# Kernel tuning notes

Hardware: AMD Instinct MI355X
Metric: run time of the kernel (lower is better)

Reference implementation:

```python
import jax, jax.numpy as jnp
import numpy as np

P = 64
K = 64
D = 2048
KERNEL_MUL = 2.0
KERNEL_NUM = 5


def setup_inputs() -> dict:
    key = jax.random.key(0)
    k1, k2 = jax.random.split(key)
    source = jax.random.normal(k1, (P * K, D), dtype=jnp.float32)
    target = jax.random.normal(k2, (P * K, D), dtype=jnp.float32)
    return {"source": source, "target": target}


def _mmd_terms(source, target):
    # split into P groups of K rows each, process all splits at once
    src = source.reshape(P, K, D)
    tgt = target.reshape(P, K, D)
    total = jnp.concatenate([src, tgt], axis=1)          # [P, 2K, D]
    n = 2 * K
    # pairwise squared L2 distances per split: [P, 2K, 2K]
    sq = jnp.sum(total * total, axis=-1)                  # [P, 2K]
    gram = jnp.einsum('pid,pjd->pij', total, total)       # [P, 2K, 2K]
    l2 = sq[:, :, None] + sq[:, None, :] - 2.0 * gram
    # bandwidth from detached distances (torch uses L2_distance.data)
    bw = jax.lax.stop_gradient(jnp.sum(l2, axis=(1, 2))) / (n * n - n)  # [P]
    bw = bw / (KERNEL_MUL ** (KERNEL_NUM // 2))
    mults = KERNEL_MUL ** jnp.arange(KERNEL_NUM, dtype=jnp.float32)     # [kn]
    bws = bw[:, None] * mults[None, :] + 1e-9                           # [P, kn]
    # multi-bandwidth Gaussian kernel sum: [P, 2K, 2K]
    kern = jnp.sum(jnp.exp(-l2[:, None, :, :] / bws[:, :, None, None]), axis=1)
    XX = kern[:, :K, :K]
    YY = kern[:, K:, K:]
    XY = kern[:, :K, K:]
    YX = kern[:, K:, :K]
    xx = jnp.mean(XX, axis=(1, 2))
    yy = jnp.mean(YY, axis=(1, 2))
    xy = jnp.mean(XY, axis=(1, 2))
    yx = jnp.mean(YX, axis=(1, 2))
    per_split_loss = xx + yy - xy - yx                    # [P]
    total_loss = jnp.sum(per_split_loss) / P
    return total_loss, l2, xx, yy, xy, yx


def reference(source, target):
    total_loss, l2, xx, yy, xy, yx = _mmd_terms(source, target)
    # original returns max of l2dist from the LAST split only
    max_l2_last = jnp.max(l2[-1])
    return (total_loss.reshape(1), max_l2_last,
            jnp.sum(xx) / P, jnp.sum(yy) / P, jnp.sum(xy) / P, jnp.sum(yx) / P)
```

## Files before the change

### kernel.cpp

```cpp
#include <hip/hip_runtime.h>

typedef _Float16 half8 __attribute__((ext_vector_type(8)));
typedef float floatx4 __attribute__((ext_vector_type(4)));
typedef unsigned int uint2v __attribute__((ext_vector_type(2)));

#define NSPLIT 64
#define KS 64
#define DIM 2048
#define NROW 128
#define BK 128
#define KSPL 8
#define KCH (DIM / KSPL)
#define NKC_A (KCH / BK)
#define SST 152
#define GSZ (NROW * NROW)
#define GT_OFF (NSPLIT * KSPL * GSZ)

__device__ __forceinline__ unsigned int pk16(float a, float b) {
  return __builtin_bit_cast(unsigned int, __builtin_amdgcn_cvt_pkrtz(a, b));
}

__global__ void init_kernel(float* out, float* ws) {
  if (threadIdx.x < 6) out[threadIdx.x] = 0.0f;
  if (threadIdx.x < NSPLIT) ws[GT_OFF + threadIdx.x] = 0.0f;
}

__global__ __launch_bounds__(1024) void gram_kernel(const float* __restrict__ src,
                                                    const float* __restrict__ tgt,
                                                    float* __restrict__ ws) {
  __shared__ __align__(16) _Float16 stage[NROW * SST];
  __shared__ float red[16];

  const int p = blockIdx.x >> 3;
  const int c = blockIdx.x & (KSPL - 1);
  const int tid = threadIdx.x;
  const int lane = tid & 63;
  const int wave = tid >> 6;

  const int srow = tid >> 3;
  const int c4 = (tid & 7) * 4;
  const float* rowp = ((srow < KS) ? (src + (size_t)(p * KS + srow) * DIM)
                                   : (tgt + (size_t)(p * KS + (srow - KS)) * DIM)) +
                      c * KCH;

  const int wr = (wave >> 2) * 32;
  const int wc = (wave & 3) * 32;
  const int fr = lane & 15;
  const int fk = (lane >> 4) * 8;

  floatx4 acc00 = {0.f, 0.f, 0.f, 0.f};
  floatx4 acc01 = {0.f, 0.f, 0.f, 0.f};
  floatx4 acc10 = {0.f, 0.f, 0.f, 0.f};
  floatx4 acc11 = {0.f, 0.f, 0.f, 0.f};

  float4 f0, f1, f2, f3;
#define LOADK(kc)                                      \
  do {                                                 \
    const float* gp_ = rowp + (kc) * BK + c4;          \
    f0 = *(const float4*)(gp_);                        \
    f1 = *(const float4*)(gp_ + 32);                   \
    f2 = *(const float4*)(gp_ + 64);                   \
    f3 = *(const float4*)(gp_ + 96);                   \
  } while (0)

  LOADK(0);
  for (int kc = 0; kc < NKC_A; ++kc) {
    __syncthreads();
    {
      _Float16* sp = &stage[srow * SST + c4];
      *(uint2v*)(sp)      = (uint2v){pk16(f0.x, f0.y), pk16(f0.z, f0.w)};
      *(uint2v*)(sp + 32) = (uint2v){pk16(f1.x, f1.y), pk16(f1.z, f1.w)};
      *(uint2v*)(sp + 64) = (uint2v){pk16(f2.x, f2.y), pk16(f2.z, f2.w)};
      *(uint2v*)(sp + 96) = (uint2v){pk16(f3.x, f3.y), pk16(f3.z, f3.w)};
    }
    __syncthreads();
    if (kc + 1 < NKC_A) LOADK(kc + 1);
#pragma unroll
    for (int ks = 0; ks < 4; ++ks) {
      const int ko = ks * 32 + fk;
      half8 a0 = *(const half8*)&stage[(wr + fr) * SST + ko];
      half8 a1 = *(const half8*)&stage[(wr + 16 + fr) * SST + ko];
      half8 b0 = *(const half8*)&stage[(wc + fr) * SST + ko];
      half8 b1 = *(const half8*)&stage[(wc + 16 + fr) * SST + ko];
      acc00 = __builtin_amdgcn_mfma_f32_16x16x32_f16(a0, b0, acc00, 0, 0, 0);
      acc01 = __builtin_amdgcn_mfma_f32_16x16x32_f16(a0, b1, acc01, 0, 0, 0);
      acc10 = __builtin_amdgcn_mfma_f32_16x16x32_f16(a1, b0, acc10, 0, 0, 0);
      acc11 = __builtin_amdgcn_mfma_f32_16x16x32_f16(a1, b1, acc11, 0, 0, 0);
    }
  }
#undef LOADK

  float* wsp = ws + (size_t)blockIdx.x * GSZ;
  const int ccol = lane & 15;
  const int crow = (lane >> 4) * 4;
  float gsum = 0.0f;
#pragma unroll
  for (int r = 0; r < 4; ++r) {
    wsp[(wr + crow + r) * NROW + (wc + ccol)] = acc00[r];
    wsp[(wr + crow + r) * NROW + (wc + 16 + ccol)] = acc01[r];
    wsp[(wr + 16 + crow + r) * NROW + (wc + ccol)] = acc10[r];
    wsp[(wr + 16 + crow + r) * NROW + (wc + 16 + ccol)] = acc11[r];
    gsum += acc00[r] + acc01[r] + acc10[r] + acc11[r];
  }
#pragma unroll
  for (int m = 1; m <= 32; m <<= 1) gsum += __shfl_xor(gsum, m, 64);
  if (lane == 0) red[wave] = gsum;
  __syncthreads();
  if (tid == 0) {
    float t = 0.0f;
    for (int w = 0; w < 16; ++w) t += red[w];
    atomicAdd(&ws[GT_OFF + p], t);
  }
}

__global__ __launch_bounds__(1024) void reduce_kernel(const float* __restrict__ ws,
                                                      float* __restrict__ out) {
  __shared__ float sqv[NROW];
  __shared__ float bcast[8];
  __shared__ float redm[16];
  __shared__ float quad2[2];

  const int p = blockIdx.x >> 2;
  const int rb = blockIdx.x & 3;
  const int tid = threadIdx.x;
  const int lane = tid & 63;
  const int wave = tid >> 6;

  const int lr = tid >> 5;
  const int cg = tid & 31;
  const int row = rb * 32 + lr;

  const float* base = ws + (size_t)(p * KSPL) * GSZ + row * NROW + cg * 4;
  float4 g = {0.f, 0.f, 0.f, 0.f};
#pragma unroll
  for (int c8 = 0; c8 < KSPL; ++c8) {
    float4 t = *(const float4*)(base + (size_t)c8 * GSZ);
    g.x += t.x; g.y += t.y; g.z += t.z; g.w += t.w;
  }

  if (tid < NROW) {
    const float* dp = ws + (size_t)(p * KSPL) * GSZ + tid * (NROW + 1);
    float d = 0.0f;
#pragma unroll
    for (int c8 = 0; c8 < KSPL; ++c8) d += dp[(size_t)c8 * GSZ];
    sqv[tid] = d;
  }
  if (tid < 2) quad2[tid] = 0.0f;
  __syncthreads();

  if (tid == 0) {
    float ssq = 0.0f;
    for (int i = 0; i < NROW; ++i) ssq += sqv[i];
    float gt = ws[GT_OFF + p];
    float suml2 = 2.0f * (float)NROW * ssq - 2.0f * gt;
    float bw = suml2 / (float)(NROW * NROW - NROW) * 0.25f;
    float mult = 1.0f;
    for (int k = 0; k < 5; ++k) {
      bcast[k] = 1.0f / (bw * mult + 1e-9f);
      mult *= 2.0f;
    }
  }
  __syncthreads();

  const float sqi = sqv[row];
  float l2r[4];
  float lmax = 0.0f;
#pragma unroll
  for (int k = 0; k < 4; ++k) {
    float v = sqi + sqv[cg * 4 + k] - 2.0f * ((const float*)&g)[k];
    l2r[k] = v;
    lmax = fmaxf(lmax, v);
  }

  if (p == NSPLIT - 1) {
#pragma unroll
    for (int m = 1; m <= 32; m <<= 1) lmax = fmaxf(lmax, __shfl_xor(lmax, m, 64));
    if (lane == 0) redm[wave] = lmax;
    __syncthreads();
    if (tid == 0) {
      float mx = 0.0f;
      for (int w = 0; w < 16; ++w) mx = fmaxf(mx, redm[w]);
      atomicMax((int*)(out + 1), __float_as_int(mx));
    }
  }

  const float ib0 = bcast[0], ib1 = bcast[1], ib2 = bcast[2], ib3 = bcast[3], ib4 = bcast[4];
  float qsum = 0.0f;
#pragma unroll
  for (int k = 0; k < 4; ++k) {
    float v = l2r[k];
    qsum += __expf(-v * ib0) + __expf(-v * ib1) + __expf(-v * ib2) +
            __expf(-v * ib3) + __expf(-v * ib4);
  }
  qsum += __shfl_xor(qsum, 1, 64);
  qsum += __shfl_xor(qsum, 2, 64);
  qsum += __shfl_xor(qsum, 4, 64);
  qsum += __shfl_xor(qsum, 8, 64);
  qsum += __shfl_xor(qsum, 32, 64);
  if (lane == 0) atomicAdd(&quad2[0], qsum);
  if (lane == 16) atomicAdd(&quad2[1], qsum);
  __syncthreads();

  if (tid == 0) {
    const float inv = 1.0f / (4096.0f * 64.0f);
    float qx = quad2[0], qy = quad2[1];
    if (rb < 2) {
      atomicAdd(&out[0], (qx - qy) * inv);
      atomicAdd(&out[2], qx * inv);
      atomicAdd(&out[4], qy * inv);
    } else {
      atomicAdd(&out[0], (qy - qx) * inv);
      atomicAdd(&out[3], qy * inv);
      atomicAdd(&out[5], qx * inv);
    }
  }
}

extern "C" void kernel_launch(void* const* d_in, const int* in_sizes, int n_in,
                              void* d_out, int out_size, void* d_ws, size_t ws_size,
                              hipStream_t stream) {
  const float* src = (const float*)d_in[0];
  const float* tgt = (const float*)d_in[1];
  float* out = (float*)d_out;
  float* ws = (float*)d_ws;
  init_kernel<<<1, 64, 0, stream>>>(out, ws);
  gram_kernel<<<NSPLIT * KSPL, 1024, 0, stream>>>(src, tgt, ws);
  reduce_kernel<<<NSPLIT * 4, 1024, 0, stream>>>(ws, out);
}
```

Baseline: 123.0 us.

## Halve K-split count and issue all global loads upfront per block

Cuts the number of K-split chunks per split from 8 to 4, so each gram block covers 512 columns (4 k-chunks), and the reduce kernel sums fewer partial Gram matrices. All four chunks' global loads are now issued at once into registers before the compute loop, replacing one-ahead prefetching, so more memory requests are in flight. Register pressure rises, so the launch-bounds hint asks for 4 blocks per CU, and the grid shrinks to 256 blocks, which may underfill the GPU.

After: 116.6 us. -5.2%, faster.

```diff
diff --git a/kernel.cpp b/kernel.cpp
--- a/kernel.cpp
+++ b/kernel.cpp
@@ -9,7 +9,7 @@
 #define DIM 2048
 #define NROW 128
 #define BK 128
-#define KSPL 8
+#define KSPL 4
 #define KCH (DIM / KSPL)
 #define NKC_A (KCH / BK)
 #define SST 152
@@ -25,13 +25,13 @@
   if (threadIdx.x < NSPLIT) ws[GT_OFF + threadIdx.x] = 0.0f;
 }
 
-__global__ __launch_bounds__(1024) void gram_kernel(const float* __restrict__ src,
-                                                    const float* __restrict__ tgt,
-                                                    float* __restrict__ ws) {
+__global__ __launch_bounds__(1024, 4) void gram_kernel(const float* __restrict__ src,
+                                                       const float* __restrict__ tgt,
+                                                       float* __restrict__ ws) {
   __shared__ __align__(16) _Float16 stage[NROW * SST];
   __shared__ float red[16];
 
-  const int p = blockIdx.x >> 3;
+  const int p = blockIdx.x >> 2;
   const int c = blockIdx.x & (KSPL - 1);
   const int tid = threadIdx.x;
   const int lane = tid & 63;
@@ -53,28 +53,27 @@
   floatx4 acc10 = {0.f, 0.f, 0.f, 0.f};
   floatx4 acc11 = {0.f, 0.f, 0.f, 0.f};
 
-  float4 f0, f1, f2, f3;
-#define LOADK(kc)                                      \
-  do {                                                 \
-    const float* gp_ = rowp + (kc) * BK + c4;          \
-    f0 = *(const float4*)(gp_);                        \
-    f1 = *(const float4*)(gp_ + 32);                   \
-    f2 = *(const float4*)(gp_ + 64);                   \
-    f3 = *(const float4*)(gp_ + 96);                   \
-  } while (0)
-
-  LOADK(0);
+  float4 f[NKC_A][4];
+#pragma unroll
+  for (int kc = 0; kc < NKC_A; ++kc) {
+    const float* gp = rowp + kc * BK + c4;
+    f[kc][0] = *(const float4*)(gp);
+    f[kc][1] = *(const float4*)(gp + 32);
+    f[kc][2] = *(const float4*)(gp + 64);
+    f[kc][3] = *(const float4*)(gp + 96);
+  }
+
+#pragma unroll
   for (int kc = 0; kc < NKC_A; ++kc) {
     __syncthreads();
     {
       _Float16* sp = &stage[srow * SST + c4];
-      *(uint2v*)(sp)      = (uint2v){pk16(f0.x, f0.y), pk16(f0.z, f0.w)};
-      *(uint2v*)(sp + 32) = (uint2v){pk16(f1.x, f1.y), pk16(f1.z, f1.w)};
-      *(uint2v*)(sp + 64) = (uint2v){pk16(f2.x, f2.y), pk16(f2.z, f2.w)};
-      *(uint2v*)(sp + 96) = (uint2v){pk16(f3.x, f3.y), pk16(f3.z, f3.w)};
+      *(uint2v*)(sp)      = (uint2v){pk16(f[kc][0].x, f[kc][0].y), pk16(f[kc][0].z, f[kc][0].w)};
+      *(uint2v*)(sp + 32) = (uint2v){pk16(f[kc][1].x, f[kc][1].y), pk16(f[kc][1].z, f[kc][1].w)};
+      *(uint2v*)(sp + 64) = (uint2v){pk16(f[kc][2].x, f[kc][2].y), pk16(f[kc][2].z, f[kc][2].w)};
+      *(uint2v*)(sp + 96) = (uint2v){pk16(f[kc][3].x, f[kc][3].y), pk16(f[kc][3].z, f[kc][3].w)};
     }
     __syncthreads();
-    if (kc + 1 < NKC_A) LOADK(kc + 1);
 #pragma unroll
     for (int ks = 0; ks < 4; ++ks) {
       const int ko = ks * 32 + fk;
@@ -88,7 +87,6 @@
       acc11 = __builtin_amdgcn_mfma_f32_16x16x32_f16(a1, b1, acc11, 0, 0, 0);
     }
   }
-#undef LOADK
 
   float* wsp = ws + (size_t)blockIdx.x * GSZ;
   const int ccol = lane & 15;
```

## Halve K-split partials, store MFMA fragments natively, replace atomics with final reduction

Applied to the files above, without the earlier changes.

The K-split of the Gram computation drops from 8 to 4, which halves the partial Gram matrices written to and read back from workspace. Accumulators are now stored in their native MFMA fragment layout as vector stores, and the reduce kernel gathers them with remapped indices. The init kernel and all global atomics are replaced by per-block partial records and a small final kernel that reduces them deterministically. The trade-off is fewer gram blocks with longer K loops (256 blocks of 1024 threads), plus strided scalar gathers in the reduce kernel.

Result: faster. 109.5 us (-11.0%).

```diff
diff --git a/kernel.cpp b/kernel.cpp
--- a/kernel.cpp
+++ b/kernel.cpp
@@ -9,20 +9,18 @@
 #define DIM 2048
 #define NROW 128
 #define BK 128
-#define KSPL 8
+#define KSPL 4
 #define KCH (DIM / KSPL)
 #define NKC_A (KCH / BK)
 #define SST 152
 #define GSZ (NROW * NROW)
-#define GT_OFF (NSPLIT * KSPL * GSZ)
+#define NBLK (NSPLIT * KSPL)
+#define GT2_OFF (NBLK * GSZ)
+#define PART_OFF (GT2_OFF + NBLK)
+
 
 __device__ __forceinline__ unsigned int pk16(float a, float b) {
   return __builtin_bit_cast(unsigned int, __builtin_amdgcn_cvt_pkrtz(a, b));
-}
-
-__global__ void init_kernel(float* out, float* ws) {
-  if (threadIdx.x < 6) out[threadIdx.x] = 0.0f;
-  if (threadIdx.x < NSPLIT) ws[GT_OFF + threadIdx.x] = 0.0f;
 }
 
 __global__ __launch_bounds__(1024) void gram_kernel(const float* __restrict__ src,
@@ -31,7 +29,7 @@
   __shared__ __align__(16) _Float16 stage[NROW * SST];
   __shared__ float red[16];
 
-  const int p = blockIdx.x >> 3;
+  const int p = blockIdx.x >> 2;
   const int c = blockIdx.x & (KSPL - 1);
   const int tid = threadIdx.x;
   const int lane = tid & 63;
@@ -90,18 +88,15 @@
   }
 #undef LOADK
 
-  float* wsp = ws + (size_t)blockIdx.x * GSZ;
-  const int ccol = lane & 15;
-  const int crow = (lane >> 4) * 4;
+  float* wsp = ws + (size_t)blockIdx.x * GSZ + wave * 1024 + lane * 4;
+  *(floatx4*)(wsp)       = acc00;
+  *(floatx4*)(wsp + 256) = acc01;
+  *(floatx4*)(wsp + 512) = acc10;
+  *(floatx4*)(wsp + 768) = acc11;
+
   float gsum = 0.0f;
 #pragma unroll
-  for (int r = 0; r < 4; ++r) {
-    wsp[(wr + crow + r) * NROW + (wc + ccol)] = acc00[r];
-    wsp[(wr + crow + r) * NROW + (wc + 16 + ccol)] = acc01[r];
-    wsp[(wr + 16 + crow + r) * NROW + (wc + ccol)] = acc10[r];
-    wsp[(wr + 16 + crow + r) * NROW + (wc + 16 + ccol)] = acc11[r];
-    gsum += acc00[r] + acc01[r] + acc10[r] + acc11[r];
-  }
+  for (int r = 0; r < 4; ++r) gsum += acc00[r] + acc01[r] + acc10[r] + acc11[r];
 #pragma unroll
   for (int m = 1; m <= 32; m <<= 1) gsum += __shfl_xor(gsum, m, 64);
   if (lane == 0) red[wave] = gsum;
@@ -109,7 +104,7 @@
   if (tid == 0) {
     float t = 0.0f;
     for (int w = 0; w < 16; ++w) t += red[w];
-    atomicAdd(&ws[GT_OFF + p], t);
+    ws[GT2_OFF + blockIdx.x] = t;
   }
 }
 
@@ -120,30 +115,39 @@
   __shared__ float redm[16];
   __shared__ float quad2[2];
 
-  const int p = blockIdx.x >> 2;
-  const int rb = blockIdx.x & 3;
+  const int b = blockIdx.x;
+  const int p = b >> 2;
+  const int rb = b & 3;
   const int tid = threadIdx.x;
   const int lane = tid & 63;
   const int wave = tid >> 6;
 
-  const int lr = tid >> 5;
+  const int row = rb * 32 + (tid >> 5);
   const int cg = tid & 31;
-  const int row = rb * 32 + lr;
-
-  const float* base = ws + (size_t)(p * KSPL) * GSZ + row * NROW + cg * 4;
-  float4 g = {0.f, 0.f, 0.f, 0.f};
+
+  const float* sb = ws + (size_t)(p * KSPL) * GSZ;
+  const int wv = ((row >> 5) << 2) + (cg >> 3);
+  const int a = (((row >> 4) & 1) << 1) + ((cg >> 2) & 1);
+  const int ln = (((row & 15) >> 2) << 4) + ((cg & 3) << 2);
+  const int idx = wv * 1024 + a * 256 + ln * 4 + (row & 3);
+
+  float g0 = 0.f, g1 = 0.f, g2 = 0.f, g3 = 0.f;
 #pragma unroll
   for (int c8 = 0; c8 < KSPL; ++c8) {
-    float4 t = *(const float4*)(base + (size_t)c8 * GSZ);
-    g.x += t.x; g.y += t.y; g.z += t.z; g.w += t.w;
+    const float* bp = sb + (size_t)c8 * GSZ + idx;
+    g0 += bp[0]; g1 += bp[4]; g2 += bp[8]; g3 += bp[12];
   }
 
   if (tid < NROW) {
-    const float* dp = ws + (size_t)(p * KSPL) * GSZ + tid * (NROW + 1);
+    const int i = tid;
+    const int wd = (i >> 5) * 5;
+    const int ad = ((i >> 4) & 1) * 3;
+    const int lnd = (((i & 15) >> 2) << 4) + (i & 15);
+    const int idxd = wd * 1024 + ad * 256 + lnd * 4 + (i & 3);
     float d = 0.0f;
 #pragma unroll
-    for (int c8 = 0; c8 < KSPL; ++c8) d += dp[(size_t)c8 * GSZ];
-    sqv[tid] = d;
+    for (int c8 = 0; c8 < KSPL; ++c8) d += sb[(size_t)c8 * GSZ + idxd];
+    sqv[i] = d;
   }
   if (tid < 2) quad2[tid] = 0.0f;
   __syncthreads();
@@ -151,7 +155,8 @@
   if (tid == 0) {
     float ssq = 0.0f;
     for (int i = 0; i < NROW; ++i) ssq += sqv[i];
-    float gt = ws[GT_OFF + p];
+    float gt = ws[GT2_OFF + p * 4 + 0] + ws[GT2_OFF + p * 4 + 1] +
+               ws[GT2_OFF + p * 4 + 2] + ws[GT2_OFF + p * 4 + 3];
     float suml2 = 2.0f * (float)NROW * ssq - 2.0f * gt;
     float bw = suml2 / (float)(NROW * NROW - NROW) * 0.25f;
     float mult = 1.0f;
@@ -165,24 +170,18 @@
   const float sqi = sqv[row];
   float l2r[4];
   float lmax = 0.0f;
-#pragma unroll
-  for (int k = 0; k < 4; ++k) {
-    float v = sqi + sqv[cg * 4 + k] - 2.0f * ((const float*)&g)[k];
-    l2r[k] = v;
-    lmax = fmaxf(lmax, v);
-  }
-
-  if (p == NSPLIT - 1) {
-#pragma unroll
-    for (int m = 1; m <= 32; m <<= 1) lmax = fmaxf(lmax, __shfl_xor(lmax, m, 64));
-    if (lane == 0) redm[wave] = lmax;
-    __syncthreads();
-    if (tid == 0) {
-      float mx = 0.0f;
-      for (int w = 0; w < 16; ++w) mx = fmaxf(mx, redm[w]);
-      atomicMax((int*)(out + 1), __float_as_int(mx));
-    }
-  }
+  {
+    const float gg[4] = {g0, g1, g2, g3};
+#pragma unroll
+    for (int k = 0; k < 4; ++k) {
+      float v = sqi + sqv[cg * 4 + k] - 2.0f * gg[k];
+      l2r[k] = v;
+      lmax = fmaxf(lmax, v);
+    }
+  }
+#pragma unroll
+  for (int m = 1; m <= 32; m <<= 1) lmax = fmaxf(lmax, __shfl_xor(lmax, m, 64));
+  if (lane == 0) redm[wave] = lmax;
 
   const float ib0 = bcast[0], ib1 = bcast[1], ib2 = bcast[2], ib3 = bcast[3], ib4 = bcast[4];
   float qsum = 0.0f;
@@ -202,17 +201,52 @@
   __syncthreads();
 
   if (tid == 0) {
+    float mx = 0.0f;
+    for (int w = 0; w < 16; ++w) mx = fmaxf(mx, redm[w]);
+    float4* part = (float4*)(ws + PART_OFF);
+    part[b] = make_float4(quad2[0], quad2[1], mx, 0.0f);
+  }
+}
+
+__global__ __launch_bounds__(256) void final_kernel(const float* __restrict__ ws,
+                                                    float* __restrict__ out) {
+  __shared__ float fr[4][5];
+  const int tid = threadIdx.x;
+  const int lane = tid & 63;
+  const int wave = tid >> 6;
+  const float4* part = (const float4*)(ws + PART_OFF);
+  float4 pt = part[tid];
+  const int rb = tid & 3;
+  float xx = (rb < 2) ? pt.x : 0.0f;
+  float xy = (rb < 2) ? pt.y : 0.0f;
+  float yx = (rb >= 2) ? pt.x : 0.0f;
+  float yy = (rb >= 2) ? pt.y : 0.0f;
+  float mx = ((tid >> 2) == NSPLIT - 1) ? pt.z : 0.0f;
+#pragma unroll
+  for (int m = 1; m <= 32; m <<= 1) {
+    xx += __shfl_xor(xx, m, 64);
+    xy += __shfl_xor(xy, m, 64);
+    yx += __shfl_xor(yx, m, 64);
+    yy += __shfl_xor(yy, m, 64);
+    mx = fmaxf(mx, __shfl_xor(mx, m, 64));
+  }
+  if (lane == 0) {
+    fr[wave][0] = xx; fr[wave][1] = xy; fr[wave][2] = yx; fr[wave][3] = yy; fr[wave][4] = mx;
+  }
+  __syncthreads();
+  if (tid == 0) {
+    float sxx = 0, sxy = 0, syx = 0, syy = 0, smx = 0;
+    for (int w = 0; w < 4; ++w) {
+      sxx += fr[w][0]; sxy += fr[w][1]; syx += fr[w][2]; syy += fr[w][3];
+      smx = fmaxf(smx, fr[w][4]);
+    }
     const float inv = 1.0f / (4096.0f * 64.0f);
-    float qx = quad2[0], qy = quad2[1];
-    if (rb < 2) {
-      atomicAdd(&out[0], (qx - qy) * inv);
-      atomicAdd(&out[2], qx * inv);
-      atomicAdd(&out[4], qy * inv);
-    } else {
-      atomicAdd(&out[0], (qy - qx) * inv);
-      atomicAdd(&out[3], qy * inv);
-      atomicAdd(&out[5], qx * inv);
-    }
+    out[0] = (sxx + syy - sxy - syx) * inv;
+    out[1] = smx;
+    out[2] = sxx * inv;
+    out[3] = syy * inv;
+    out[4] = sxy * inv;
+    out[5] = syx * inv;
   }
 }
 
@@ -223,7 +257,7 @@
   const float* tgt = (const float*)d_in[1];
   float* out = (float*)d_out;
   float* ws = (float*)d_ws;
-  init_kernel<<<1, 64, 0, stream>>>(out, ws);
-  gram_kernel<<<NSPLIT * KSPL, 1024, 0, stream>>>(src, tgt, ws);
-  reduce_kernel<<<NSPLIT * 4, 1024, 0, stream>>>(ws, out);
-}
+  gram_kernel<<<NBLK, 1024, 0, stream>>>(src, tgt, ws);
+  reduce_kernel<<<NBLK, 1024, 0, stream>>>(ws, out);
+  final_kernel<<<1, 256, 0, stream>>>(ws, out);
+}
```
